# Kernel tuning notes

Hardware: AMD Instinct MI355X
Metric: run time of the kernel (lower is better)

Reference implementation:

```python
import jax, jax.numpy as jnp
import numpy as np

GAMMA = 0.1   # gl.gamma
BIG = 1e10    # stand-in for +inf in the DP border (keeps grads NaN-free)


def _softdtw(D, gamma=GAMMA):
    """Soft-DTW value for a batch of cost matrices D: [B, T, T] -> [B].
    R[i,j] = D[i,j] + softmin_gamma(R[i-1,j-1], R[i-1,j], R[i,j-1]).
    Vectorized over the batch; sequential DP over rows (outer scan) and
    columns (inner scan), matching the reference recurrence exactly.
    """
    B, T, _ = D.shape
    dt = D.dtype
    # R[0, :] = [0, inf, inf, ...]  (length T+1, padded border)
    prev = jnp.concatenate([jnp.zeros((B, 1), dt), jnp.full((B, T), BIG, dt)], axis=1)

    def col_step(r_left, xs):
        d, r_diag, r_up = xs  # each [B]
        stacked = jnp.stack([r_diag, r_up, r_left])  # [3, B]
        r = d - gamma * jax.nn.logsumexp(-stacked / gamma, axis=0)
        return r, r

    def row_step(prev_row, d_row):  # prev_row [B, T+1], d_row [B, T]
        xs = (d_row.T, prev_row[:, :-1].T, prev_row[:, 1:].T)  # each [T, B]
        _, rows = jax.lax.scan(col_step, jnp.full((B,), BIG, dt), xs)  # [T, B]
        new_row = jnp.concatenate([jnp.full((B, 1), BIG, dt), rows.T], axis=1)
        return new_row, None

    final_row, _ = jax.lax.scan(row_step, prev, jnp.swapaxes(D, 0, 1))
    return final_row[:, -1]  # R[T, T]


def setup_inputs() -> dict:
    key = jax.random.key(0)
    n_class, n_support, n_query, t, c = 20, 5, 25, 32, 2048
    n = n_class * (n_support + n_query)
    inp = jax.random.normal(key, (n, t, c), jnp.float32)
    # episode labels, grouped per class (as produced by an episodic sampler)
    target = jnp.repeat(jnp.arange(n_class, dtype=jnp.int32), n_support + n_query)
    return {"inp": inp, "target": target, "n_support": n_support, "n_class": n_class}


def reference(inp, target, n_support, n_class):
    n, t, c = inp.shape
    per_class = n // n_class
    n_query = per_class - n_support

    # group samples by class (stable sort == torch.nonzero(target.eq(c)) ordering)
    order = jnp.argsort(target, stable=True)
    grouped = inp[order].reshape(n_class, per_class, t, c)
    z_proto = grouped[:, :n_support].mean(axis=1)                 # [m, t, c]
    zq = grouped[:, n_support:].reshape(n_class * n_query, t, c)  # [nq, t, c]

    # pairwise squared-Euclidean frame costs (no [nq*m, t, c] expansion)
    x2 = jnp.sum(zq * zq, axis=-1)          # [nq, t]
    y2 = jnp.sum(z_proto * z_proto, axis=-1)  # [m, t]
    xy = jnp.einsum('nic,mjc->nmij', zq, z_proto)  # [nq, m, t, t]
    cost_xy = x2[:, None, :, None] + y2[None, :, None, :] - 2.0 * xy
    nq, m = cost_xy.shape[:2]
    d_xy = _softdtw(cost_xy.reshape(nq * m, t, t)).reshape(nq, m)

    # normalization terms: D(x,x), D(y,y)
    cxx = x2[:, :, None] + x2[:, None, :] - 2.0 * jnp.einsum('nic,njc->nij', zq, zq)
    cyy = y2[:, :, None] + y2[:, None, :] - 2.0 * jnp.einsum('mic,mjc->mij', z_proto, z_proto)
    d_xx = _softdtw(cxx)  # [nq]
    d_yy = _softdtw(cyy)  # [m]
    dist = d_xy - 0.5 * (d_xx[:, None] + d_yy[None, :])  # [nq, m]

    log_p_y = jax.nn.log_softmax(-dist, axis=1).reshape(n_class, n_query, n_class)
    tgt = jnp.broadcast_to(jnp.arange(n_class)[:, None, None], (n_class, n_query, 1))
    batch_loss = -jnp.take_along_axis(log_p_y, tgt, axis=2).reshape(-1)
    loss_val = batch_loss.mean()
    y_hat = jnp.argmax(log_p_y, axis=2)
    acc_val = (y_hat == tgt[..., 0]).astype(jnp.float32).mean()
    return loss_val, acc_val, batch_loss
```

## Files before the change

kernel.cpp:

```cpp
#include <hip/hip_runtime.h>

#define T 32
#define C 2048
#define NTOT 600
#define NCLASS 20
#define NSUP 5
#define PER 30
#define NQPC 25
#define NQ 500
#define NQROWS (NQ * T)
#define NPROWS (NCLASS * T)
#define GAMMA 0.1f
#define INVG 10.0f
#define BIG 1e10f
#define NMM (NQ * NCLASS + NQ + NCLASS)
#define GEMM_BLKS 625
#define SYRK_BLKS_PAD 136
#define SAMP_STRIDE 8192
#define STAGE_BLKS_A 2400
#define STAGE_BLKS_B 80
#define LDS_PITCH 33

typedef __fp16 half8 __attribute__((ext_vector_type(8)));
typedef __fp16 half4 __attribute__((ext_vector_type(4)));
typedef float f32x4 __attribute__((ext_vector_type(4)));

__global__ __launch_bounds__(640) void sort_kernel(const int* __restrict__ target,
                                                   int* __restrict__ order,
                                                   int* __restrict__ qsrc) {
    __shared__ int tgt[NTOT];
    __shared__ int offs[NCLASS];
    __shared__ int ordl[NTOT];
    int tid = threadIdx.x;
    if (tid < NTOT) tgt[tid] = target[tid];
    __syncthreads();
    if (tid < NCLASS) {
        int o = 0;
        for (int i = 0; i < NTOT; i++) o += (tgt[i] < tid) ? 1 : 0;
        offs[tid] = o;
    }
    __syncthreads();
    if (tid < NTOT) {
        int c = tgt[tid];
        int rank = 0;
        for (int k = 0; k < NTOT; k++) rank += (k < tid && tgt[k] == c) ? 1 : 0;
        ordl[offs[c] + rank] = tid;
    }
    __syncthreads();
    if (tid < NTOT) order[tid] = ordl[tid];
    if (tid < NQ) qsrc[tid] = ordl[(tid / NQPC) * PER + NSUP + (tid % NQPC)];
}

__global__ __launch_bounds__(256) void stage_kernel(const float* __restrict__ inp,
                                                    const int* __restrict__ order,
                                                    half8* __restrict__ Ah,
                                                    half8* __restrict__ Bh) {
    __shared__ half8 lds[4][16][LDS_PITCH];
    int tid = threadIdx.x;
    int lane = tid & 63, w = tid >> 6;
    int bid = blockIdx.x;
    bool isA = bid < STAGE_BLKS_A;
    int b = isA ? bid : bid - STAGE_BLKS_A;
    int rowblk = b >> 1, half = b & 1;
    int row0 = rowblk * 16;
    int colbase = half * 1024 + w * 256;
    if (isA) {
        int sample = row0 >> 5, rowin0 = row0 & 31;
        const float* sbase = inp + (size_t)sample * (T * C) + (size_t)rowin0 * C +
                             colbase + lane * 4;
#pragma unroll
        for (int rr = 0; rr < 16; rr++) {
            float4 v = *(const float4*)(sbase + (size_t)rr * C);
            half4 hv = {(__fp16)v.x, (__fp16)v.y, (__fp16)v.z, (__fp16)v.w};
            ((half4*)&lds[w][rr][0])[lane] = hv;
        }
        __syncthreads();
        int chunkbase = half * 128 + w * 32;
        half8* dst = Ah + (size_t)sample * SAMP_STRIDE + rowin0;
#pragma unroll
        for (int c = 0; c < 8; c++) {
            int idx = c * 64 + lane;
            int ch = idx >> 4, row = idx & 15;
            dst[(size_t)(chunkbase + ch) * 32 + row] = lds[w][row][ch];
        }
    } else {
#pragma unroll
        for (int rr = 0; rr < 16; rr++) {
            int rg = row0 + rr;
            int cls = rg >> 5, trow = rg & 31;
            const float* base = inp + (size_t)trow * C + colbase + lane * 4;
            float4 a = *(const float4*)(base + (size_t)order[cls * PER + 0] * (T * C));
            float4 b4 = *(const float4*)(base + (size_t)order[cls * PER + 1] * (T * C));
            float4 c = *(const float4*)(base + (size_t)order[cls * PER + 2] * (T * C));
            float4 d = *(const float4*)(base + (size_t)order[cls * PER + 3] * (T * C));
            float4 e = *(const float4*)(base + (size_t)order[cls * PER + 4] * (T * C));
            float4 m;
            m.x = (a.x + b4.x + c.x + d.x + e.x) * 0.2f;
            m.y = (a.y + b4.y + c.y + d.y + e.y) * 0.2f;
            m.z = (a.z + b4.z + c.z + d.z + e.z) * 0.2f;
            m.w = (a.w + b4.w + c.w + d.w + e.w) * 0.2f;
            half4 hv = {(__fp16)m.x, (__fp16)m.y, (__fp16)m.z, (__fp16)m.w};
            ((half4*)&lds[w][rr][0])[lane] = hv;
        }
        __syncthreads();
        int chunkbase = half * 128 + w * 32;
#pragma unroll
        for (int c = 0; c < 8; c++) {
            int idx = c * 64 + lane;
            int ch = idx >> 4, row = idx & 15;
            Bh[(size_t)(chunkbase + ch) * NPROWS + row0 + row] = lds[w][row][ch];
        }
    }
}

__global__ __launch_bounds__(256) void gemm_syrk_kernel(const half8* __restrict__ Ah,
                                                        const half8* __restrict__ Bh,
                                                        const int* __restrict__ qsrc,
                                                        float* __restrict__ xy,
                                                        float* __restrict__ gxx,
                                                        float* __restrict__ gyy) {
    int tid = threadIdx.x, lane = tid & 63, wid = tid >> 6;
    int o = blockIdx.x;
    int g = lane >> 4, r = lane & 15;
    if (o < SYRK_BLKS_PAD) {
        int ww = o * 4 + wid;
        if (ww >= NQ + NCLASS) return;
        f32x4 acc[2][2];
        f32x4 zero = {0.f, 0.f, 0.f, 0.f};
        acc[0][0] = zero; acc[0][1] = zero; acc[1][0] = zero; acc[1][1] = zero;
        if (ww < NQ) {
            const half8* p = Ah + (size_t)qsrc[ww] * SAMP_STRIDE + g * 32 + r;
            float* outp = gxx + (size_t)ww * (T * T);
            for (int t = 0; t < C / 32; t++) {
                half8 h0 = p[0], h1 = p[16];
                p += 128;
                acc[0][0] = __builtin_amdgcn_mfma_f32_16x16x32_f16(h0, h0, acc[0][0], 0, 0, 0);
                acc[0][1] = __builtin_amdgcn_mfma_f32_16x16x32_f16(h0, h1, acc[0][1], 0, 0, 0);
                acc[1][0] = __builtin_amdgcn_mfma_f32_16x16x32_f16(h1, h0, acc[1][0], 0, 0, 0);
                acc[1][1] = __builtin_amdgcn_mfma_f32_16x16x32_f16(h1, h1, acc[1][1], 0, 0, 0);
            }
#pragma unroll
            for (int mi = 0; mi < 2; mi++)
#pragma unroll
                for (int ni = 0; ni < 2; ni++)
#pragma unroll
                    for (int j = 0; j < 4; j++)
                        outp[(mi * 16 + g * 4 + j) * T + ni * 16 + r] = acc[mi][ni][j];
        } else {
            int row0 = (ww - NQ) * 32;
            float* outp = gyy + (size_t)(ww - NQ) * (T * T);
            for (int t = 0; t < C / 32; t++) {
                size_t base = (size_t)(t * 4 + g) * NPROWS + row0 + r;
                half8 h0 = Bh[base], h1 = Bh[base + 16];
                acc[0][0] = __builtin_amdgcn_mfma_f32_16x16x32_f16(h0, h0, acc[0][0], 0, 0, 0);
                acc[0][1] = __builtin_amdgcn_mfma_f32_16x16x32_f16(h0, h1, acc[0][1], 0, 0, 0);
                acc[1][0] = __builtin_amdgcn_mfma_f32_16x16x32_f16(h1, h0, acc[1][0], 0, 0, 0);
                acc[1][1] = __builtin_amdgcn_mfma_f32_16x16x32_f16(h1, h1, acc[1][1], 0, 0, 0);
            }
#pragma unroll
            for (int mi = 0; mi < 2; mi++)
#pragma unroll
                for (int ni = 0; ni < 2; ni++)
#pragma unroll
                    for (int j = 0; j < 4; j++)
                        outp[(mi * 16 + g * 4 + j) * T + ni * 16 + r] = acc[mi][ni][j];
        }
        return;
    }
    int oo = o - SYRK_BLKS_PAD;
    int xcd = oo & 7, slot = oo >> 3;
    int v = (xcd < 1 ? xcd * 79 : 79 + (xcd - 1) * 78) + slot;
    int bm = v / 5, bn = v % 5;
    int wr = wid >> 1, wc = wid & 1;
    int m0 = bm * 128 + wr * 64, n0 = bn * 128 + wc * 64;
    int q0 = m0 >> 5;
    const half8* pA0 = Ah + (size_t)qsrc[q0] * SAMP_STRIDE + g * 32 + r;
    const half8* pA1 = Ah + (size_t)qsrc[q0 + 1] * SAMP_STRIDE + g * 32 + r;
    const half8* pB = Bh + (size_t)g * NPROWS + n0 + r;
    f32x4 acc[4][4];
    f32x4 zero = {0.f, 0.f, 0.f, 0.f};
#pragma unroll
    for (int mi = 0; mi < 4; mi++)
#pragma unroll
        for (int ni = 0; ni < 4; ni++) acc[mi][ni] = zero;
#pragma unroll 2
    for (int t = 0; t < C / 32; t++) {
        half8 ah[4], bh[4];
        ah[0] = pA0[0];
        ah[1] = pA0[16];
        ah[2] = pA1[0];
        ah[3] = pA1[16];
#pragma unroll
        for (int i = 0; i < 4; i++) bh[i] = pB[i * 16];
        pA0 += 128;
        pA1 += 128;
        pB += 4 * NPROWS;
#pragma unroll
        for (int mi = 0; mi < 4; mi++)
#pragma unroll
            for (int ni = 0; ni < 4; ni++)
                acc[mi][ni] = __builtin_amdgcn_mfma_f32_16x16x32_f16(ah[mi], bh[ni], acc[mi][ni], 0, 0, 0);
    }
    int orow = m0 + g * 4;
    int ocol = n0 + r;
#pragma unroll
    for (int mi = 0; mi < 4; mi++)
#pragma unroll
        for (int ni = 0; ni < 4; ni++)
#pragma unroll
            for (int j = 0; j < 4; j++)
                xy[(size_t)(orow + mi * 16 + j) * NPROWS + ocol + ni * 16] = acc[mi][ni][j];
}

__global__ void diag_kernel(const float* __restrict__ gxx, const float* __restrict__ gyy,
                            float* __restrict__ x2, float* __restrict__ y2) {
    int i = blockIdx.x * 256 + threadIdx.x;
    if (i < NQROWS) {
        x2[i] = gxx[(size_t)(i >> 5) * (T * T) + (i & 31) * (T + 1)];
    } else if (i < NQROWS + NPROWS) {
        int j = i - NQROWS;
        y2[j] = gyy[(size_t)(j >> 5) * (T * T) + (j & 31) * (T + 1)];
    }
}

__global__ __launch_bounds__(256) void softdtw_wave_kernel(
        const float* __restrict__ xy, const float* __restrict__ gxx,
        const float* __restrict__ gyy, const float* __restrict__ x2,
        const float* __restrict__ y2, float* __restrict__ dxy,
        float* __restrict__ dxx, float* __restrict__ dyy) {
    int tid = threadIdx.x;
    int j = tid & 31;
    int mm = blockIdx.x * 8 + (tid >> 5);
    bool valid = mm < NMM;
    int mmc = valid ? mm : 0;
    const float* rterm;
    const float* cterm;
    const float* cptr;
    int cstride;
    float* outp;
    if (mmc < NQ * NCLASS) {
        int q = mmc / NCLASS, m = mmc % NCLASS;
        rterm = x2 + q * T;
        cterm = y2 + m * T;
        cptr = xy + (size_t)(q * T) * NPROWS + m * T;
        cstride = NPROWS;
        outp = dxy + mmc;
    } else if (mmc < NQ * NCLASS + NQ) {
        int i = mmc - NQ * NCLASS;
        rterm = x2 + i * T;
        cterm = rterm;
        cptr = gxx + (size_t)i * (T * T);
        cstride = T;
        outp = dxx + i;
    } else {
        int i = mmc - NQ * NCLASS - NQ;
        rterm = y2 + i * T;
        cterm = rterm;
        cptr = gyy + (size_t)i * (T * T);
        cstride = T;
        outp = dyy + i;
    }
    float cjv = cterm[j];
    float xreg = rterm[j];
    float my_prev = BIG, my_prev2 = BIG;
    int ip = 0 - j; ip = ip < 0 ? 0 : (ip > 31 ? 31 : ip);
    float nxt_xy = cptr[(size_t)ip * cstride + j];
    for (int k = 0; k < 63; k++) {
        float cur_xy = nxt_xy;
        int in = k + 1 - j; in = in < 0 ? 0 : (in > 31 ? 31 : in);
        nxt_xy = cptr[(size_t)in * cstride + j];
        float lp = __shfl_up(my_prev, 1, 32);
        float dg = __shfl_up(my_prev2, 1, 32);
        if (j == 0) { lp = BIG; dg = (k == 0) ? 0.f : BIG; }
        float up = my_prev;
        int i = k - j;
        float ai = __shfl(xreg, i & 31, 32);
        float d = ai + cjv - 2.0f * cur_xy;
        float mn = fminf(dg, fminf(up, lp));
        float ssum = __expf((mn - dg) * INVG) + __expf((mn - up) * INVG) +
                     __expf((mn - lp) * INVG);
        float r = d + mn - GAMMA * __logf(ssum);
        bool active = (i >= 0) && (i < 32);
        my_prev2 = my_prev;
        my_prev = active ? r : my_prev;
    }
    if (j == 31 && valid) *outp = my_prev;
}

__global__ __launch_bounds__(512) void finalize_kernel(const float* __restrict__ dxy,
                                                       const float* __restrict__ dxx,
                                                       const float* __restrict__ dyy,
                                                       float* __restrict__ out) {
    __shared__ float sl[512];
    __shared__ float sa[512];
    int q = threadIdx.x;
    float bl = 0.f, fl = 0.f;
    if (q < NQ) {
        float dxxq = dxx[q];
        int cq = q / NQPC;
        float dd[NCLASS];
#pragma unroll
        for (int m = 0; m < NCLASS; m++)
            dd[m] = dxy[q * NCLASS + m] - 0.5f * (dxxq + dyy[m]);
        float best = dd[0];
        int bi = 0;
#pragma unroll
        for (int m = 1; m < NCLASS; m++) {
            if (dd[m] < best) { best = dd[m]; bi = m; }
        }
        float s = 0.f;
        float dcq = dd[0];
#pragma unroll
        for (int m = 0; m < NCLASS; m++) {
            s += __expf(best - dd[m]);
            if (m == cq) dcq = dd[m];
        }
        float lse = __logf(s) - best;
        bl = dcq + lse;
        out[2 + q] = bl;
        fl = (bi == cq) ? 1.f : 0.f;
    }
    sl[threadIdx.x] = bl;
    sa[threadIdx.x] = fl;
    __syncthreads();
    for (int off = 256; off; off >>= 1) {
        if (threadIdx.x < off) {
            sl[threadIdx.x] += sl[threadIdx.x + off];
            sa[threadIdx.x] += sa[threadIdx.x + off];
        }
        __syncthreads();
    }
    if (threadIdx.x == 0) {
        out[0] = sl[0] / (float)NQ;
        out[1] = sa[0] / (float)NQ;
    }
}

extern "C" void kernel_launch(void* const* d_in, const int* in_sizes, int n_in,
                              void* d_out, int out_size, void* d_ws, size_t ws_size,
                              hipStream_t stream) {
    const float* inp = (const float*)d_in[0];
    const int* target = (const int*)d_in[1];
    float* out = (float*)d_out;
    char* ws = (char*)d_ws;

    size_t off = 0;
    auto carve = [&](size_t bytes) {
        void* p = ws + off;
        off = (off + bytes + 255) & ~(size_t)255;
        return p;
    };
    int* order = (int*)carve(NTOT * sizeof(int));
    int* qsrc = (int*)carve(NQ * sizeof(int));
    float* x2 = (float*)carve((size_t)NQROWS * sizeof(float));
    float* y2 = (float*)carve((size_t)NPROWS * sizeof(float));
    float* xy = (float*)carve((size_t)NQROWS * NPROWS * sizeof(float));
    float* gxx = (float*)carve((size_t)NQ * T * T * sizeof(float));
    float* gyy = (float*)carve((size_t)NCLASS * T * T * sizeof(float));
    float* dxy = (float*)carve((size_t)NQ * NCLASS * sizeof(float));
    float* dxx = (float*)carve((size_t)NQ * sizeof(float));
    float* dyy = (float*)carve((size_t)NCLASS * sizeof(float));
    half8* Ah = (half8*)carve((size_t)NTOT * SAMP_STRIDE * 16);
    half8* Bh = (half8*)carve((size_t)(C / 8) * NPROWS * 16);
    (void)ws_size;

    sort_kernel<<<1, 640, 0, stream>>>(target, order, qsrc);
    stage_kernel<<<STAGE_BLKS_A + STAGE_BLKS_B, 256, 0, stream>>>(inp, order, Ah, Bh);
    gemm_syrk_kernel<<<SYRK_BLKS_PAD + GEMM_BLKS, 256, 0, stream>>>(Ah, Bh, qsrc, xy, gxx, gyy);
    diag_kernel<<<(NQROWS + NPROWS + 255) / 256, 256, 0, stream>>>(gxx, gyy, x2, y2);
    softdtw_wave_kernel<<<(NMM + 7) / 8, 256, 0, stream>>>(xy, gxx, gyy, x2, y2, dxy, dxx, dyy);
    finalize_kernel<<<1, 512, 0, stream>>>(dxy, dxx, dyy, out);
}
```

Measured before the change: 178.1 us.

## Stage only query samples into Ah and read diagonal norms from Gram directly

The staging kernel now converts only the 500 query samples, gathered through qsrc, instead of all 600 samples. This skips the fp16 conversion and stores for the 100 support samples, which were never read from Ah. The GEMM/SYRK kernels index Ah directly by query index, so the per-wave qsrc lookups go away. The separate diag kernel that extracted x2/y2 is removed, and the soft-DTW kernel reads the diagonals straight from the Gram matrices, saving one launch and one round trip through global memory.

New measurement: 173.9 us. 2.4% less time.

```diff
diff --git a/kernel.cpp b/kernel.cpp
--- a/kernel.cpp
+++ b/kernel.cpp
@@ -17,7 +17,7 @@
 #define GEMM_BLKS 625
 #define SYRK_BLKS_PAD 136
 #define SAMP_STRIDE 8192
-#define STAGE_BLKS_A 2400
+#define STAGE_BLKS_A 2000
 #define STAGE_BLKS_B 80
 #define LDS_PITCH 33
 
@@ -52,6 +52,7 @@
 }
 
 __global__ __launch_bounds__(256) void stage_kernel(const float* __restrict__ inp,
+                                                    const int* __restrict__ qsrc,
                                                     const int* __restrict__ order,
                                                     half8* __restrict__ Ah,
                                                     half8* __restrict__ Bh) {
@@ -65,8 +66,8 @@
     int row0 = rowblk * 16;
     int colbase = half * 1024 + w * 256;
     if (isA) {
-        int sample = row0 >> 5, rowin0 = row0 & 31;
-        const float* sbase = inp + (size_t)sample * (T * C) + (size_t)rowin0 * C +
+        int q = row0 >> 5, rowin0 = row0 & 31;
+        const float* sbase = inp + (size_t)qsrc[q] * (T * C) + (size_t)rowin0 * C +
                              colbase + lane * 4;
 #pragma unroll
         for (int rr = 0; rr < 16; rr++) {
@@ -76,7 +77,7 @@
         }
         __syncthreads();
         int chunkbase = half * 128 + w * 32;
-        half8* dst = Ah + (size_t)sample * SAMP_STRIDE + rowin0;
+        half8* dst = Ah + (size_t)q * SAMP_STRIDE + rowin0;
 #pragma unroll
         for (int c = 0; c < 8; c++) {
             int idx = c * 64 + lane;
@@ -115,7 +116,6 @@
 
 __global__ __launch_bounds__(256) void gemm_syrk_kernel(const half8* __restrict__ Ah,
                                                         const half8* __restrict__ Bh,
-                                                        const int* __restrict__ qsrc,
                                                         float* __restrict__ xy,
                                                         float* __restrict__ gxx,
                                                         float* __restrict__ gyy) {
@@ -129,7 +129,7 @@
         f32x4 zero = {0.f, 0.f, 0.f, 0.f};
         acc[0][0] = zero; acc[0][1] = zero; acc[1][0] = zero; acc[1][1] = zero;
         if (ww < NQ) {
-            const half8* p = Ah + (size_t)qsrc[ww] * SAMP_STRIDE + g * 32 + r;
+            const half8* p = Ah + (size_t)ww * SAMP_STRIDE + g * 32 + r;
             float* outp = gxx + (size_t)ww * (T * T);
             for (int t = 0; t < C / 32; t++) {
                 half8 h0 = p[0], h1 = p[16];
@@ -174,8 +174,8 @@
     int wr = wid >> 1, wc = wid & 1;
     int m0 = bm * 128 + wr * 64, n0 = bn * 128 + wc * 64;
     int q0 = m0 >> 5;
-    const half8* pA0 = Ah + (size_t)qsrc[q0] * SAMP_STRIDE + g * 32 + r;
-    const half8* pA1 = Ah + (size_t)qsrc[q0 + 1] * SAMP_STRIDE + g * 32 + r;
+    const half8* pA0 = Ah + (size_t)q0 * SAMP_STRIDE + g * 32 + r;
+    const half8* pA1 = pA0 + SAMP_STRIDE;
     const half8* pB = Bh + (size_t)g * NPROWS + n0 + r;
     f32x4 acc[4][4];
     f32x4 zero = {0.f, 0.f, 0.f, 0.f};
@@ -212,56 +212,44 @@
                 xy[(size_t)(orow + mi * 16 + j) * NPROWS + ocol + ni * 16] = acc[mi][ni][j];
 }
 
-__global__ void diag_kernel(const float* __restrict__ gxx, const float* __restrict__ gyy,
-                            float* __restrict__ x2, float* __restrict__ y2) {
-    int i = blockIdx.x * 256 + threadIdx.x;
-    if (i < NQROWS) {
-        x2[i] = gxx[(size_t)(i >> 5) * (T * T) + (i & 31) * (T + 1)];
-    } else if (i < NQROWS + NPROWS) {
-        int j = i - NQROWS;
-        y2[j] = gyy[(size_t)(j >> 5) * (T * T) + (j & 31) * (T + 1)];
-    }
-}
-
 __global__ __launch_bounds__(256) void softdtw_wave_kernel(
         const float* __restrict__ xy, const float* __restrict__ gxx,
-        const float* __restrict__ gyy, const float* __restrict__ x2,
-        const float* __restrict__ y2, float* __restrict__ dxy,
+        const float* __restrict__ gyy, float* __restrict__ dxy,
         float* __restrict__ dxx, float* __restrict__ dyy) {
     int tid = threadIdx.x;
     int j = tid & 31;
     int mm = blockIdx.x * 8 + (tid >> 5);
     bool valid = mm < NMM;
     int mmc = valid ? mm : 0;
-    const float* rterm;
-    const float* cterm;
+    const float* rbase;
+    const float* cbase;
     const float* cptr;
     int cstride;
     float* outp;
     if (mmc < NQ * NCLASS) {
         int q = mmc / NCLASS, m = mmc % NCLASS;
-        rterm = x2 + q * T;
-        cterm = y2 + m * T;
+        rbase = gxx + (size_t)q * (T * T);
+        cbase = gyy + (size_t)m * (T * T);
         cptr = xy + (size_t)(q * T) * NPROWS + m * T;
         cstride = NPROWS;
         outp = dxy + mmc;
     } else if (mmc < NQ * NCLASS + NQ) {
         int i = mmc - NQ * NCLASS;
-        rterm = x2 + i * T;
-        cterm = rterm;
-        cptr = gxx + (size_t)i * (T * T);
+        rbase = gxx + (size_t)i * (T * T);
+        cbase = rbase;
+        cptr = rbase;
         cstride = T;
         outp = dxx + i;
     } else {
         int i = mmc - NQ * NCLASS - NQ;
-        rterm = y2 + i * T;
-        cterm = rterm;
-        cptr = gyy + (size_t)i * (T * T);
+        rbase = gyy + (size_t)i * (T * T);
+        cbase = rbase;
+        cptr = rbase;
         cstride = T;
         outp = dyy + i;
     }
-    float cjv = cterm[j];
-    float xreg = rterm[j];
+    float cjv = cbase[j * 33];
+    float xreg = rbase[j * 33];
     float my_prev = BIG, my_prev2 = BIG;
     int ip = 0 - j; ip = ip < 0 ? 0 : (ip > 31 ? 31 : ip);
     float nxt_xy = cptr[(size_t)ip * cstride + j];
@@ -352,22 +340,19 @@
     };
     int* order = (int*)carve(NTOT * sizeof(int));
     int* qsrc = (int*)carve(NQ * sizeof(int));
-    float* x2 = (float*)carve((size_t)NQROWS * sizeof(float));
-    float* y2 = (float*)carve((size_t)NPROWS * sizeof(float));
     float* xy = (float*)carve((size_t)NQROWS * NPROWS * sizeof(float));
     float* gxx = (float*)carve((size_t)NQ * T * T * sizeof(float));
     float* gyy = (float*)carve((size_t)NCLASS * T * T * sizeof(float));
     float* dxy = (float*)carve((size_t)NQ * NCLASS * sizeof(float));
     float* dxx = (float*)carve((size_t)NQ * sizeof(float));
     float* dyy = (float*)carve((size_t)NCLASS * sizeof(float));
-    half8* Ah = (half8*)carve((size_t)NTOT * SAMP_STRIDE * 16);
+    half8* Ah = (half8*)carve((size_t)NQ * SAMP_STRIDE * 16);
     half8* Bh = (half8*)carve((size_t)(C / 8) * NPROWS * 16);
     (void)ws_size;
 
     sort_kernel<<<1, 640, 0, stream>>>(target, order, qsrc);
-    stage_kernel<<<STAGE_BLKS_A + STAGE_BLKS_B, 256, 0, stream>>>(inp, order, Ah, Bh);
-    gemm_syrk_kernel<<<SYRK_BLKS_PAD + GEMM_BLKS, 256, 0, stream>>>(Ah, Bh, qsrc, xy, gxx, gyy);
-    diag_kernel<<<(NQROWS + NPROWS + 255) / 256, 256, 0, stream>>>(gxx, gyy, x2, y2);
-    softdtw_wave_kernel<<<(NMM + 7) / 8, 256, 0, stream>>>(xy, gxx, gyy, x2, y2, dxy, dxx, dyy);
+    stage_kernel<<<STAGE_BLKS_A + STAGE_BLKS_B, 256, 0, stream>>>(inp, qsrc, order, Ah, Bh);
+    gemm_syrk_kernel<<<SYRK_BLKS_PAD + GEMM_BLKS, 256, 0, stream>>>(Ah, Bh, xy, gxx, gyy);
+    softdtw_wave_kernel<<<(NMM + 7) / 8, 256, 0, stream>>>(xy, gxx, gyy, dxy, dxx, dyy);
     finalize_kernel<<<1, 512, 0, stream>>>(dxy, dxx, dyy, out);
 }
```
